# Optimization experiments

Measured on AMD Instinct MI355X. Metric: run time of the kernel, lower is better.

The kernel has to match this reference:

```python
import jax, jax.numpy as jnp
import numpy as np

U, I, T, D, A = 100000, 50000, 512, 64, 64
B, RU, RI = 2048, 50, 50


def _xavier(key, shape):
    fan_in, fan_out = shape[0], shape[1]
    lim = jnp.sqrt(6.0 / (fan_in + fan_out)).astype(jnp.float32)
    return jax.random.uniform(key, shape, jnp.float32, -lim, lim)


def setup_inputs() -> dict:
    key = jax.random.key(0)
    ks = jax.random.split(key, 16)
    return {
        "user": jax.random.randint(ks[0], (B,), 0, U),
        "item": jax.random.randint(ks[1], (B,), 0, I),
        "user_r_topic": jax.random.uniform(ks[2], (B, RU, T), jnp.float32),
        "item_r_topic": jax.random.uniform(ks[3], (B, RI, T), jnp.float32),
        "user_embed_w": 0.05 * jax.random.normal(ks[4], (U, D), jnp.float32),
        "item_embed_w": 0.05 * jax.random.normal(ks[5], (I, D), jnp.float32),
        "user_att_w": 0.05 * jax.random.normal(ks[6], (U, D), jnp.float32),
        "item_att_w": 0.05 * jax.random.normal(ks[7], (I, D), jnp.float32),
        "topic_embed_w": 0.05 * jax.random.normal(ks[8], (T, D), jnp.float32),
        "fc_u_w": _xavier(ks[9], (D, A)), "fc_u_b": jnp.zeros((A,), jnp.float32),
        "fc_ru_w": _xavier(ks[10], (D, A)), "fc_ru_b": jnp.zeros((A,), jnp.float32),
        "fc_i_w": _xavier(ks[11], (D, A)), "fc_i_b": jnp.zeros((A,), jnp.float32),
        "fc_ri_w": _xavier(ks[12], (D, A)), "fc_ri_b": jnp.zeros((A,), jnp.float32),
        "h_u_w": _xavier(ks[13], (A, 1)), "h_u_b": jnp.zeros((1,), jnp.float32),
        "h_i_w": _xavier(ks[14], (A, 1)), "h_i_b": jnp.zeros((1,), jnp.float32),
        "fc_pre_w": _xavier(ks[15], (2 * D, 1)), "fc_pre_b": jnp.zeros((1,), jnp.float32),
    }


def _branch(ids, emb_w, att_w, r_topic, topic_w, fc_a_w, fc_a_b, fc_r_w, fc_r_b, h_w, h_b):
    # embedding lookups
    emb = emb_w[ids]            # [B, D]
    att = att_w[ids]            # [B, D]
    # broadcast mul + sum over topics == matmul with topic table: [B, R, D]
    review = jnp.einsum("brt,td->brd", r_topic, topic_w)
    # attention scores over reviews
    s = jax.nn.relu((att @ fc_a_w + fc_a_b)[:, None, :] + review @ fc_r_w + fc_r_b)
    w = jax.nn.softmax((s @ h_w)[..., 0] + h_b[0], axis=1)   # [B, R]
    feat = jnp.einsum("br,brd->bd", w, review)               # attention pooling
    # (feat[:,None,:] * topic_emphasize).sum(dim=1) == feat * topic_w.sum(0)
    feat = feat * jnp.sum(topic_w, axis=0)
    return emb, feat


def reference(user, item, user_r_topic, item_r_topic,
              user_embed_w, item_embed_w, user_att_w, item_att_w, topic_embed_w,
              fc_u_w, fc_u_b, fc_ru_w, fc_ru_b, fc_i_w, fc_i_b, fc_ri_w, fc_ri_b,
              h_u_w, h_u_b, h_i_w, h_i_b, fc_pre_w, fc_pre_b):
    u_emb, u_feat = _branch(user, user_embed_w, user_att_w, user_r_topic, topic_embed_w,
                            fc_u_w, fc_u_b, fc_ru_w, fc_ru_b, h_u_w, h_u_b)
    i_emb, i_feat = _branch(item, item_embed_w, item_att_w, item_r_topic, topic_embed_w,
                            fc_i_w, fc_i_b, fc_ri_w, fc_ri_b, h_i_w, h_i_b)
    tmp = jnp.concatenate([u_feat + u_emb, i_feat + i_emb], axis=1)  # [B, 2D]
    pred = jax.nn.relu(tmp @ fc_pre_w + fc_pre_b)                    # [B, 1]
    return pred[:, 0]
```

## Files before the change

kernel.cpp:

```cpp
#include <hip/hip_runtime.h>
#include <cstdint>
#include <cstddef>

#define NB 2048
#define NT 512
#define ND 64
#define NR 50
#define REVP 68

typedef __attribute__((ext_vector_type(8))) short bf16x8;
typedef __attribute__((ext_vector_type(4))) float f32x4;

__device__ inline unsigned short f2bf_rne(float x) {
    unsigned int u = __float_as_uint(x);
    u += 0x7fffu + ((u >> 16) & 1u);
    return (unsigned short)(u >> 16);
}

__device__ inline bf16x8 cvt8_rne(float4 v0, float4 v1) {
    union { unsigned int u[4]; bf16x8 v; } P;
    asm("v_cvt_pk_bf16_f32 %0, %1, %2" : "=v"(P.u[0]) : "v"(v0.x), "v"(v0.y));
    asm("v_cvt_pk_bf16_f32 %0, %1, %2" : "=v"(P.u[1]) : "v"(v0.z), "v"(v0.w));
    asm("v_cvt_pk_bf16_f32 %0, %1, %2" : "=v"(P.u[2]) : "v"(v1.x), "v"(v1.y));
    asm("v_cvt_pk_bf16_f32 %0, %1, %2" : "=v"(P.u[3]) : "v"(v1.z), "v"(v1.w));
    return P.v;
}

__device__ inline void gload16(const void* gsrc, void* ldst) {
    __builtin_amdgcn_global_load_lds(
        (const __attribute__((address_space(1))) unsigned int*)gsrc,
        (__attribute__((address_space(3))) unsigned int*)ldst, 16, 0, 0);
}

__global__ __launch_bounds__(256) void prep_kernel(
    const float* __restrict__ tw,
    const float* __restrict__ fc_u_w, const float* __restrict__ fc_ru_w,
    const float* __restrict__ fc_i_w, const float* __restrict__ fc_ri_w,
    unsigned short* __restrict__ bhi,
    unsigned short* __restrict__ fuhi, unsigned short* __restrict__ fihi)
{
    int i = blockIdx.x * 256 + threadIdx.x;
    if (i < 32768) {
        int j  = i & 7;
        int l  = (i >> 3) & 63;
        int n  = (i >> 9) & 3;
        int kk = i >> 11;
        int t = kk * 32 + ((l >> 4) << 3) + j;
        int d = n * 16 + (l & 15);
        bhi[i] = f2bf_rne(tw[t * ND + d]);
    } else {
        int q = i - 32768;
        int br = q >> 13;
        int e = q & 8191;
        int j  = e & 7;
        int l  = (e >> 3) & 63;
        int n  = (e >> 9) & 3;
        int kk = e >> 11;
        int k = kk * 32 + ((l >> 4) << 3) + j;
        int col = n * 16 + (l & 15);
        const float* W = (k < 64) ? (br ? fc_ri_w : fc_ru_w)
                                  : (br ? fc_i_w  : fc_u_w);
        unsigned short hi = f2bf_rne(W[(k & 63) * ND + col]);
        if (br) fihi[e] = hi; else fuhi[e] = hi;
    }
}

__global__ __launch_bounds__(256) void colsum_kernel(const float* __restrict__ tw,
                                                     float* __restrict__ colsum) {
    __shared__ float part[4][ND];
    int d = threadIdx.x & 63, p = threadIdx.x >> 6;
    float s = 0.f;
    for (int t = p; t < NT; t += 4) s += tw[t * ND + d];
    part[p][d] = s;
    __syncthreads();
    if (threadIdx.x < ND)
        colsum[d] = part[0][d] + part[1][d] + part[2][d] + part[3][d];
}

__global__ __launch_bounds__(256, 3) void branch_kernel(
    const int* __restrict__ user, const int* __restrict__ item,
    const float* __restrict__ user_r_topic, const float* __restrict__ item_r_topic,
    const float* __restrict__ user_embed_w, const float* __restrict__ item_embed_w,
    const float* __restrict__ user_att_w, const float* __restrict__ item_att_w,
    const unsigned short* __restrict__ bhi,
    const unsigned short* __restrict__ fuhi, const unsigned short* __restrict__ fihi,
    const float* __restrict__ fc_u_b, const float* __restrict__ fc_ru_b,
    const float* __restrict__ fc_i_b, const float* __restrict__ fc_ri_b,
    const float* __restrict__ h_u_w, const float* __restrict__ h_u_b,
    const float* __restrict__ h_i_w, const float* __restrict__ h_i_b,
    const float* __restrict__ colsum,
    float* __restrict__ u_vec, float* __restrict__ i_vec)
{
    __shared__ __align__(16) unsigned char blds[32768];
    __shared__ float rev[NR][REVP];
    __shared__ float lds_logit[NR + 2];

    const int tid = threadIdx.x, wave = tid >> 6, lane = tid & 63;
    const int g = lane >> 4, c16 = lane & 15;

    const int bb = blockIdx.x;
    const int branch = bb >> 11;
    const int b = bb & (NB - 1);

    const int*   ids     = branch ? item           : user;
    const float* r_topic = branch ? item_r_topic   : user_r_topic;
    const float* emb_w   = branch ? item_embed_w   : user_embed_w;
    const float* att_w   = branch ? item_att_w     : user_att_w;
    const unsigned short* fhi = branch ? fihi : fuhi;
    const float* fc_a_b  = branch ? fc_i_b         : fc_u_b;
    const float* fc_r_b  = branch ? fc_ri_b        : fc_ru_b;
    const float* h_w     = branch ? h_i_w          : h_u_w;
    const float* h_b     = branch ? h_i_b          : h_u_b;
    float*       out_vec = branch ? i_vec          : u_vec;

    const int id = ids[b];
    const int rowm = wave * 16 + c16;
    const int rowc = rowm < NR ? rowm : NR - 1;
    const float* arow = r_topic + (size_t)b * NR * NT + (size_t)rowc * NT + g * 8;

    auto stageB = [&](int h) {
        const unsigned char* src = (const unsigned char*)bhi + (size_t)h * 32768;
#pragma unroll
        for (int i = 0; i < 8; ++i) {
            size_t off = (size_t)(i * 256 + tid) * 16;
            gload16(src + off, blds + off);
        }
    };

    f32x4 acc[4];
#pragma unroll
    for (int n = 0; n < 4; ++n) acc[n] = (f32x4){0.f, 0.f, 0.f, 0.f};

    auto kstep2 = [&](int kk) {
        float4 a00 = *reinterpret_cast<const float4*>(arow + kk * 32);
        float4 a01 = *reinterpret_cast<const float4*>(arow + kk * 32 + 4);
        float4 a10 = *reinterpret_cast<const float4*>(arow + kk * 32 + 32);
        float4 a11 = *reinterpret_cast<const float4*>(arow + kk * 32 + 36);
        bf16x8 f0 = cvt8_rne(a00, a01);
        bf16x8 f1 = cvt8_rne(a10, a11);
        const int k0 = (kk & 7) * 4, k1 = ((kk + 1) & 7) * 4;
#pragma unroll
        for (int n = 0; n < 4; ++n) {
            bf16x8 b0 = *reinterpret_cast<const bf16x8*>(
                blds + (size_t)((k0 + n) * 64 + lane) * 16);
            acc[n] = __builtin_amdgcn_mfma_f32_16x16x32_bf16(f0, b0, acc[n], 0, 0, 0);
        }
#pragma unroll
        for (int n = 0; n < 4; ++n) {
            bf16x8 b1 = *reinterpret_cast<const bf16x8*>(
                blds + (size_t)((k1 + n) * 64 + lane) * 16);
            acc[n] = __builtin_amdgcn_mfma_f32_16x16x32_bf16(f1, b1, acc[n], 0, 0, 0);
        }
    };

    stageB(0);
    __syncthreads();

#pragma unroll
    for (int kk = 0; kk < 8; kk += 2) kstep2(kk);

    __syncthreads();
    stageB(1);
    __syncthreads();

#pragma unroll
    for (int kk = 8; kk < 16; kk += 2) kstep2(kk);

#pragma unroll
    for (int n = 0; n < 4; ++n)
#pragma unroll
        for (int r4 = 0; r4 < 4; ++r4) {
            int r = wave * 16 + g * 4 + r4;
            if (r < NR) rev[r][n * 16 + c16] = acc[n][r4];
        }

    f32x4 s4[4];
#pragma unroll
    for (int n = 0; n < 4; ++n) s4[n] = (f32x4){0.f, 0.f, 0.f, 0.f};

#pragma unroll
    for (int kk2 = 0; kk2 < 4; ++kk2) {
        bf16x8 bh[4];
#pragma unroll
        for (int n = 0; n < 4; ++n)
            bh[n] = *(reinterpret_cast<const bf16x8*>(fhi + (size_t)(kk2 * 4 + n) * 512) + lane);
        bf16x8 ah;
        if (kk2 < 2) {
            const float* rp = &rev[rowc][kk2 * 32 + g * 8];
            ah = cvt8_rne(*reinterpret_cast<const float4*>(rp),
                          *reinterpret_cast<const float4*>(rp + 4));
        } else {
            const float* ap = att_w + (size_t)id * ND + (kk2 - 2) * 32 + g * 8;
            ah = cvt8_rne(*reinterpret_cast<const float4*>(ap),
                          *reinterpret_cast<const float4*>(ap + 4));
        }
#pragma unroll
        for (int n = 0; n < 4; ++n)
            s4[n] = __builtin_amdgcn_mfma_f32_16x16x32_bf16(ah, bh[n], s4[n], 0, 0, 0);
    }

    const float hb = h_b[0];
    float p0 = 0.f, p1 = 0.f, p2 = 0.f, p3 = 0.f;
#pragma unroll
    for (int n = 0; n < 4; ++n) {
        float hwn = h_w[n * 16 + c16];
        float bs = fc_r_b[n * 16 + c16] + fc_a_b[n * 16 + c16];
        p0 = fmaf(fmaxf(s4[n][0] + bs, 0.f), hwn, p0);
        p1 = fmaf(fmaxf(s4[n][1] + bs, 0.f), hwn, p1);
        p2 = fmaf(fmaxf(s4[n][2] + bs, 0.f), hwn, p2);
        p3 = fmaf(fmaxf(s4[n][3] + bs, 0.f), hwn, p3);
    }
#pragma unroll
    for (int off = 1; off < 16; off <<= 1) {
        p0 += __shfl_xor(p0, off);
        p1 += __shfl_xor(p1, off);
        p2 += __shfl_xor(p2, off);
        p3 += __shfl_xor(p3, off);
    }
    if (c16 == 0) {
        int rb = wave * 16 + g * 4;
        if (rb + 0 < NR) lds_logit[rb + 0] = p0 + hb;
        if (rb + 1 < NR) lds_logit[rb + 1] = p1 + hb;
        if (rb + 2 < NR) lds_logit[rb + 2] = p2 + hb;
        if (rb + 3 < NR) lds_logit[rb + 3] = p3 + hb;
    }
    __syncthreads();

    if (wave == 0) {
        float m = -1e30f;
        for (int r = 0; r < NR; ++r) m = fmaxf(m, lds_logit[r]);
        float sum = 0.f;
        for (int r = 0; r < NR; ++r) sum += __expf(lds_logit[r] - m);
        float inv = 1.f / sum;
        float feat = 0.f;
        for (int r = 0; r < NR; ++r)
            feat = fmaf(__expf(lds_logit[r] - m), rev[r][lane], feat);
        feat *= inv;
        out_vec[(size_t)b * ND + lane] = feat * colsum[lane] + emb_w[(size_t)id * ND + lane];
    }
}

__global__ __launch_bounds__(64) void final_kernel(
    const float* __restrict__ u_vec, const float* __restrict__ i_vec,
    const float* __restrict__ fc_pre_w, const float* __restrict__ fc_pre_b,
    float* __restrict__ out)
{
    int b = blockIdx.x, lane = threadIdx.x;
    float v = u_vec[(size_t)b * ND + lane] * fc_pre_w[lane]
            + i_vec[(size_t)b * ND + lane] * fc_pre_w[ND + lane];
#pragma unroll
    for (int off = 32; off; off >>= 1) v += __shfl_xor(v, off);
    if (lane == 0) out[b] = fmaxf(v + fc_pre_b[0], 0.f);
}

extern "C" void kernel_launch(void* const* d_in, const int* in_sizes, int n_in,
                              void* d_out, int out_size, void* d_ws, size_t ws_size,
                              hipStream_t stream) {
    (void)in_sizes; (void)n_in; (void)out_size; (void)ws_size;

    const int*   user         = (const int*)d_in[0];
    const int*   item         = (const int*)d_in[1];
    const float* user_r_topic = (const float*)d_in[2];
    const float* item_r_topic = (const float*)d_in[3];
    const float* user_embed_w = (const float*)d_in[4];
    const float* item_embed_w = (const float*)d_in[5];
    const float* user_att_w   = (const float*)d_in[6];
    const float* item_att_w   = (const float*)d_in[7];
    const float* topic_w      = (const float*)d_in[8];
    const float* fc_u_w       = (const float*)d_in[9];
    const float* fc_u_b       = (const float*)d_in[10];
    const float* fc_ru_w      = (const float*)d_in[11];
    const float* fc_ru_b      = (const float*)d_in[12];
    const float* fc_i_w       = (const float*)d_in[13];
    const float* fc_i_b       = (const float*)d_in[14];
    const float* fc_ri_w      = (const float*)d_in[15];
    const float* fc_ri_b      = (const float*)d_in[16];
    const float* h_u_w        = (const float*)d_in[17];
    const float* h_u_b        = (const float*)d_in[18];
    const float* h_i_w        = (const float*)d_in[19];
    const float* h_i_b        = (const float*)d_in[20];
    const float* fc_pre_w     = (const float*)d_in[21];
    const float* fc_pre_b     = (const float*)d_in[22];

    unsigned short* bhi  = (unsigned short*)d_ws;
    unsigned short* fuhi = bhi + 32768;
    unsigned short* fihi = fuhi + 8192;
    float* colsum = (float*)(fihi + 8192);
    float* u_vec  = colsum + 64;
    float* i_vec  = u_vec + NB * ND;

    prep_kernel<<<192, 256, 0, stream>>>(topic_w, fc_u_w, fc_ru_w, fc_i_w, fc_ri_w,
                                         bhi, fuhi, fihi);
    colsum_kernel<<<1, 256, 0, stream>>>(topic_w, colsum);

    branch_kernel<<<2 * NB, 256, 0, stream>>>(
        user, item, user_r_topic, item_r_topic,
        user_embed_w, item_embed_w, user_att_w, item_att_w,
        bhi, fuhi, fihi,
        fc_u_b, fc_ru_b, fc_i_b, fc_ri_b,
        h_u_w, h_u_b, h_i_w, h_i_b,
        colsum, u_vec, i_vec);

    final_kernel<<<NB, 64, 0, stream>>>(u_vec, i_vec, fc_pre_w, fc_pre_b,
                                        (float*)d_out);
}
```

Measured before the change: 153.8 us.

## Stage review-topic rows through swizzled LDS as bf16 with coalesced loads

The review-topic A operand used to be read straight from global memory in the MFMA fragment layout, with each lane fetching strided row segments. Now each wave loads whole rows with fully coalesced float4 reads, converts them to bf16, and writes them into an XOR-swizzled LDS arena. The MFMA fragments are then read back from LDS. The rev buffer now reuses the B staging area to save space. Total LDS use grows, so launch bounds drop from 3 to 2 blocks per SM, which lowers occupancy in exchange for better global access efficiency.

```diff
diff --git a/kernel.cpp b/kernel.cpp
--- a/kernel.cpp
+++ b/kernel.cpp
@@ -7,6 +7,7 @@
 #define ND 64
 #define NR 50
 #define REVP 68
+#define ALDS 25600
 
 typedef __attribute__((ext_vector_type(8))) short bf16x8;
 typedef __attribute__((ext_vector_type(4))) float f32x4;
@@ -77,7 +78,7 @@
         colsum[d] = part[0][d] + part[1][d] + part[2][d] + part[3][d];
 }
 
-__global__ __launch_bounds__(256, 3) void branch_kernel(
+__global__ __launch_bounds__(256, 2) void branch_kernel(
     const int* __restrict__ user, const int* __restrict__ item,
     const float* __restrict__ user_r_topic, const float* __restrict__ item_r_topic,
     const float* __restrict__ user_embed_w, const float* __restrict__ item_embed_w,
@@ -91,8 +92,7 @@
     const float* __restrict__ colsum,
     float* __restrict__ u_vec, float* __restrict__ i_vec)
 {
-    __shared__ __align__(16) unsigned char blds[32768];
-    __shared__ float rev[NR][REVP];
+    __shared__ __align__(16) unsigned char arena[ALDS + 32768];
     __shared__ float lds_logit[NR + 2];
 
     const int tid = threadIdx.x, wave = tid >> 6, lane = tid & 63;
@@ -114,10 +114,28 @@
     float*       out_vec = branch ? i_vec          : u_vec;
 
     const int id = ids[b];
-    const int rowm = wave * 16 + c16;
-    const int rowc = rowm < NR ? rowm : NR - 1;
-    const float* arow = r_topic + (size_t)b * NR * NT + (size_t)rowc * NT + g * 8;
-
+    const int rowg = wave * 16 + c16;
+    const int rowc = rowg < NR ? rowg : NR - 1;
+    unsigned char* blds = arena + ALDS;
+
+    const float* Abase = r_topic + (size_t)b * NR * NT;
+
+    auto streamA = [&](int h) {
+#pragma unroll
+        for (int i = 0; i < 13; ++i) {
+            int row = i * 4 + wave;
+            if (row < NR) {
+                float4 v = *reinterpret_cast<const float4*>(
+                    Abase + (size_t)row * NT + h * 256 + lane * 4);
+                unsigned int d0, d1;
+                asm("v_cvt_pk_bf16_f32 %0, %1, %2" : "=v"(d0) : "v"(v.x), "v"(v.y));
+                asm("v_cvt_pk_bf16_f32 %0, %1, %2" : "=v"(d1) : "v"(v.z), "v"(v.w));
+                int s = lane ^ ((row & 7) << 1);
+                uint2 w2; w2.x = d0; w2.y = d1;
+                *reinterpret_cast<uint2*>(arena + row * 512 + s * 8) = w2;
+            }
+        }
+    };
     auto stageB = [&](int h) {
         const unsigned char* src = (const unsigned char*)bhi + (size_t)h * 32768;
 #pragma unroll
@@ -131,41 +149,31 @@
 #pragma unroll
     for (int n = 0; n < 4; ++n) acc[n] = (f32x4){0.f, 0.f, 0.f, 0.f};
 
-    auto kstep2 = [&](int kk) {
-        float4 a00 = *reinterpret_cast<const float4*>(arow + kk * 32);
-        float4 a01 = *reinterpret_cast<const float4*>(arow + kk * 32 + 4);
-        float4 a10 = *reinterpret_cast<const float4*>(arow + kk * 32 + 32);
-        float4 a11 = *reinterpret_cast<const float4*>(arow + kk * 32 + 36);
-        bf16x8 f0 = cvt8_rne(a00, a01);
-        bf16x8 f1 = cvt8_rne(a10, a11);
-        const int k0 = (kk & 7) * 4, k1 = ((kk + 1) & 7) * 4;
+    auto kstep = [&](int kkl) {
+        bf16x8 af = *reinterpret_cast<const bf16x8*>(
+            arena + rowc * 512 + (((kkl * 4 + g) ^ (rowc & 7)) << 4));
 #pragma unroll
         for (int n = 0; n < 4; ++n) {
-            bf16x8 b0 = *reinterpret_cast<const bf16x8*>(
-                blds + (size_t)((k0 + n) * 64 + lane) * 16);
-            acc[n] = __builtin_amdgcn_mfma_f32_16x16x32_bf16(f0, b0, acc[n], 0, 0, 0);
-        }
-#pragma unroll
-        for (int n = 0; n < 4; ++n) {
-            bf16x8 b1 = *reinterpret_cast<const bf16x8*>(
-                blds + (size_t)((k1 + n) * 64 + lane) * 16);
-            acc[n] = __builtin_amdgcn_mfma_f32_16x16x32_bf16(f1, b1, acc[n], 0, 0, 0);
+            bf16x8 bh = *reinterpret_cast<const bf16x8*>(
+                blds + (size_t)((kkl * 4 + n) * 64 + lane) * 16);
+            acc[n] = __builtin_amdgcn_mfma_f32_16x16x32_bf16(af, bh, acc[n], 0, 0, 0);
         }
     };
 
     stageB(0);
-    __syncthreads();
-
-#pragma unroll
-    for (int kk = 0; kk < 8; kk += 2) kstep2(kk);
-
+    streamA(0);
+    __syncthreads();
+#pragma unroll
+    for (int kkl = 0; kkl < 8; ++kkl) kstep(kkl);
     __syncthreads();
     stageB(1);
-    __syncthreads();
-
-#pragma unroll
-    for (int kk = 8; kk < 16; kk += 2) kstep2(kk);
-
+    streamA(1);
+    __syncthreads();
+#pragma unroll
+    for (int kkl = 0; kkl < 8; ++kkl) kstep(kkl);
+
+    __syncthreads();
+    float (*rev)[REVP] = reinterpret_cast<float(*)[REVP]>(blds);
 #pragma unroll
     for (int n = 0; n < 4; ++n)
 #pragma unroll
```

After: 176.8 us. 15.0% more time.
